# Performance work log

Measured on AMD Instinct MI355X. Metric: run time of the kernel, lower is better.

## Reference

```python
import jax, jax.numpy as jnp
import numpy as np

N, E, D = 40000, 640000, 128
EPS = 1e-5


def _lin(k, out_d, in_d):
    s = 1.0 / np.sqrt(in_d)
    kw, kb = jax.random.split(k)
    W = jax.random.uniform(kw, (out_d, in_d), minval=-s, maxval=s, dtype=jnp.float32)
    b = jax.random.uniform(kb, (out_d,), minval=-s, maxval=s, dtype=jnp.float32)
    return W, b


def setup_inputs() -> dict:
    key = jax.random.key(0)
    kx, ke, k1, k2, k3, k4 = jax.random.split(key, 6)
    x = jax.random.normal(kx, (N, D), dtype=jnp.float32)
    edge_index = jax.random.randint(ke, (2, E), 0, N, dtype=jnp.int64)
    Wm1, bm1 = _lin(k1, D, D)
    Wm2, bm2 = _lin(k2, D, D)
    Wu1, bu1 = _lin(k3, D, 2 * D)
    Wu2, bu2 = _lin(k4, D, D)
    gamma = jnp.ones((D,), jnp.float32)
    beta = jnp.zeros((D,), jnp.float32)
    return dict(x=x, edge_index=edge_index, Wm1=Wm1, bm1=bm1, Wm2=Wm2, bm2=bm2,
                Wu1=Wu1, bu1=bu1, Wu2=Wu2, bu2=bu2, gamma=gamma, beta=beta)


def reference(x, edge_index, Wm1, bm1, Wm2, bm2, Wu1, bu1, Wu2, bu2, gamma, beta):
    num_nodes = x.shape[0]
    src, dst = edge_index[0], edge_index[1]
    # message MLP on gathered source features: (E, D)
    m = jax.nn.relu(x[src] @ Wm1.T + bm1) @ Wm2.T + bm2
    # scatter-mean via segment_sum + clamped count
    agg = jax.ops.segment_sum(m, dst, num_segments=num_nodes)
    cnt = jax.ops.segment_sum(jnp.ones((dst.shape[0],), m.dtype), dst, num_segments=num_nodes)
    agg = agg / jnp.clip(cnt, 1.0, None)[:, None]
    # update MLP on concat([x, agg]) -> (N, D); dropout is identity in eval
    comb = jnp.concatenate([x, agg], axis=-1)
    u = jax.nn.relu(comb @ Wu1.T + bu1) @ Wu2.T + bu2
    # residual + LayerNorm
    h = u + x
    mu = h.mean(-1, keepdims=True)
    var = ((h - mu) ** 2).mean(-1, keepdims=True)
    return (h - mu) / jnp.sqrt(var + EPS) * gamma + beta
```

## Files before the change

kernel.cpp:

```cpp
#include <hip/hip_runtime.h>

#define N_NODES 40000
#define N_EDGES 640000
#define DIM 128
#define PAD 32
#define NBLK 625
#define SCAT_BLOCKS 625

typedef __bf16 bf16;
typedef __bf16 v8bf __attribute__((ext_vector_type(8)));
typedef __bf16 v4bf __attribute__((ext_vector_type(4)));
typedef float f32x4 __attribute__((ext_vector_type(4)));

#define MFMA(a, b, c) __builtin_amdgcn_mfma_f32_16x16x32_bf16(a, b, c, 0, 0, 0)

#define OFF_WM1 0
#define OFF_BM1 16384
#define OFF_WM2 16512
#define OFF_BM2 32896
#define OFF_WU1 33024
#define OFF_BU1 65792
#define OFF_WU2 65920
#define OFF_BU2 82304
#define OFF_GAM 82432
#define OFF_BET 82560
#define NPARAM  82688

__device__ __forceinline__ void detect(const void* x, const void* ei,
                                       int* sf, int& f32m, int& i64m) {
    const int tid = threadIdx.x;
    if (tid == 0) { sf[0] = 0; sf[1] = 0; }
    __syncthreads();
    const unsigned short* xh = (const unsigned short*)x;
    const unsigned int* eiw = (const unsigned int*)ei;
    int isf32 = 0; unsigned int orhi = 0;
    #pragma unroll
    for (int j = 0; j < 4; ++j) {
        unsigned short h = xh[2 * (tid + 256 * j)];
        if (((h >> 7) & 0xFF) >= 0xC0) isf32 = 1;
        orhi |= eiw[2 * (tid + 256 * j) + 1];
    }
    if (isf32) atomicOr(&sf[0], 1);
    if (orhi)  atomicOr(&sf[1], 1);
    __syncthreads();
    f32m = sf[0];
    i64m = sf[1] ? 0 : 1;
}

__global__ __launch_bounds__(256) void scatter_kernel(
    const void* __restrict__ x, const void* __restrict__ ei,
    const void* p0, const void* p1, const void* p2, const void* p3,
    const void* p4, const void* p5, const void* p6, const void* p7,
    const void* p8, const void* p9,
    int* __restrict__ cnt8, unsigned short* __restrict__ pad8,
    bf16* __restrict__ xb, bf16* __restrict__ wp, int* __restrict__ flags)
{
    __shared__ int sf[2];
    int f32m, i64m;
    detect(x, ei, sf, f32m, i64m);
    const int gid = blockIdx.x * 256 + threadIdx.x;
    const int gstride = SCAT_BLOCKS * 256;
    const int cls = blockIdx.x & 7;
    if (gid == 0) { flags[0] = f32m; flags[1] = i64m; }

    int s[4], d[4];
    if (i64m) {
        const long long* p = (const long long*)ei;
        int e0 = gid * 4;
        #pragma unroll
        for (int j = 0; j < 4; ++j) { s[j] = (int)p[e0 + j]; d[j] = (int)p[N_EDGES + e0 + j]; }
    } else {
        const int4* ps = (const int4*)ei;
        const int4* pd = ps + N_EDGES / 4;
        int4 sv = ps[gid], dv = pd[gid];
        s[0] = sv.x; s[1] = sv.y; s[2] = sv.z; s[3] = sv.w;
        d[0] = dv.x; d[1] = dv.y; d[2] = dv.z; d[3] = dv.w;
    }
    int pos[4];
    #pragma unroll
    for (int j = 0; j < 4; ++j) pos[j] = atomicAdd(&cnt8[cls * N_NODES + d[j]], 1);
    #pragma unroll
    for (int j = 0; j < 4; ++j)
        if (pos[j] < PAD)
            pad8[(((size_t)cls * N_NODES + d[j]) << 5) + pos[j]] = (unsigned short)s[j];

    const int NT = N_NODES * DIM;
    if (f32m) {
        const float4* g = (const float4*)x;
        v4bf* o = (v4bf*)xb;
        for (int i = gid; i < NT / 4; i += gstride) {
            float4 v = g[i];
            v4bf t; t[0] = (bf16)v.x; t[1] = (bf16)v.y; t[2] = (bf16)v.z; t[3] = (bf16)v.w;
            o[i] = t;
        }
    } else {
        const uint4* g = (const uint4*)x;
        uint4* o = (uint4*)xb;
        for (int i = gid; i < NT / 8; i += gstride) o[i] = g[i];
    }
    for (int i = gid; i < NPARAM; i += gstride) {
        const void* src; int base;
        if      (i < OFF_BM1) { src = p0; base = OFF_WM1; }
        else if (i < OFF_WM2) { src = p1; base = OFF_BM1; }
        else if (i < OFF_BM2) { src = p2; base = OFF_WM2; }
        else if (i < OFF_WU1) { src = p3; base = OFF_BM2; }
        else if (i < OFF_BU1) { src = p4; base = OFF_WU1; }
        else if (i < OFF_WU2) { src = p5; base = OFF_BU1; }
        else if (i < OFF_BU2) { src = p6; base = OFF_WU2; }
        else if (i < OFF_GAM) { src = p7; base = OFF_BU2; }
        else if (i < OFF_BET) { src = p8; base = OFF_GAM; }
        else                  { src = p9; base = OFF_BET; }
        int j = i - base;
        float v = f32m ? ((const float*)src)[j] : (float)((const bf16*)src)[j];
        wp[i] = (bf16)v;
    }
}

__global__ __launch_bounds__(256) void msg_kernel(const bf16* __restrict__ xb,
                                                  const bf16* __restrict__ wp,
                                                  bf16* __restrict__ y)
{
    __shared__ __align__(16) bf16 sc[4][16 * DIM];
    const int wave = threadIdx.x >> 6, lane = threadIdx.x & 63;
    const int l15 = lane & 15, quad = lane >> 4;
    const int row0 = (blockIdx.x * 4 + wave) * 16;
    bf16* s = sc[wave];
    const size_t ra = (size_t)(row0 + l15) * DIM;

    f32x4 acc[8] = {};
    #pragma unroll
    for (int kt = 0; kt < 4; ++kt) {
        int k0 = kt * 32 + quad * 8;
        v8bf a0 = *(const v8bf*)&xb[ra + k0];
        #pragma unroll
        for (int ct = 0; ct < 8; ++ct) {
            v8bf b = *(const v8bf*)&wp[OFF_WM1 + (size_t)(ct * 16 + l15) * DIM + k0];
            acc[ct] = MFMA(a0, b, acc[ct]);
        }
    }
    #pragma unroll
    for (int ct = 0; ct < 8; ++ct) {
        float bb = (float)wp[OFF_BM1 + ct * 16 + l15];
        int c8w = (ct << 1) | (l15 >> 3);
        #pragma unroll
        for (int r = 0; r < 4; ++r) {
            int row = quad * 4 + r;
            s[row * DIM + (((c8w ^ row) << 3) | (l15 & 7))] =
                (bf16)fmaxf(acc[ct][r] + bb, 0.f);
        }
    }
    f32x4 acc2[8] = {};
    #pragma unroll
    for (int kt = 0; kt < 4; ++kt) {
        int k0 = kt * 32 + quad * 8;
        int c8 = kt * 4 + quad;
        v8bf a0 = *(const v8bf*)&s[l15 * DIM + ((c8 ^ l15) << 3)];
        #pragma unroll
        for (int ct = 0; ct < 8; ++ct) {
            v8bf b = *(const v8bf*)&wp[OFF_WM2 + (size_t)(ct * 16 + l15) * DIM + k0];
            acc2[ct] = MFMA(a0, b, acc2[ct]);
        }
    }
    #pragma unroll
    for (int ct = 0; ct < 8; ++ct) {
        float bb = (float)wp[OFF_BM2 + ct * 16 + l15];
        #pragma unroll
        for (int r = 0; r < 4; ++r) {
            int grow = row0 + quad * 4 + r;
            y[(size_t)grow * DIM + ct * 16 + l15] = (bf16)(acc2[ct][r] + bb);
        }
    }
}

__device__ __forceinline__ void accum8(float* s, uint4 v) {
    v8bf b = __builtin_bit_cast(v8bf, v);
    #pragma unroll
    for (int j = 0; j < 8; ++j) s[j] += (float)b[j];
}

__global__ __launch_bounds__(256) void update_kernel(
    const bf16* __restrict__ xb, const bf16* __restrict__ y,
    const unsigned short* __restrict__ pad8, const int* __restrict__ cnt8,
    const bf16* __restrict__ wp, const int* __restrict__ flags,
    void* __restrict__ out)
{
    __shared__ __align__(16) bf16 sA[4][16 * DIM];
    __shared__ __align__(16) bf16 sH[4][16 * DIM];
    const int wave = threadIdx.x >> 6, lane = threadIdx.x & 63;
    const int l15 = lane & 15, quad = lane >> 4;
    const int row0 = (blockIdx.x * 4 + wave) * 16;
    bf16* sa = sA[wave];
    bf16* s  = sH[wave];
    const int of32 = flags[0];
    const uint4* yv = (const uint4*)y;

    for (int idx = 0; idx < 16; ++idx) {
        const int node = row0 + idx;
        int pref[9];
        pref[0] = 0;
        #pragma unroll
        for (int xq = 0; xq < 8; ++xq)
            pref[xq + 1] = pref[xq] + min(cnt8[xq * N_NODES + node], PAD);
        const int tot = pref[8];

        float s0[8] = {}, s1[8] = {};
        int j = quad;
        for (; j + 4 < tot; j += 8) {
            int j2 = j + 4, x1 = 0, x2 = 0;
            #pragma unroll
            for (int xq = 1; xq < 8; ++xq) {
                if (j  >= pref[xq]) x1 = xq;
                if (j2 >= pref[xq]) x2 = xq;
            }
            int i0 = pad8[(((size_t)x1 * N_NODES + node) << 5) + (j  - pref[x1])];
            int i1 = pad8[(((size_t)x2 * N_NODES + node) << 5) + (j2 - pref[x2])];
            uint4 v0 = yv[(size_t)i0 * 16 + l15];
            uint4 v1 = yv[(size_t)i1 * 16 + l15];
            accum8(s0, v0);
            accum8(s1, v1);
        }
        if (j < tot) {
            int x1 = 0;
            #pragma unroll
            for (int xq = 1; xq < 8; ++xq) if (j >= pref[xq]) x1 = xq;
            int i0 = pad8[(((size_t)x1 * N_NODES + node) << 5) + (j - pref[x1])];
            accum8(s0, yv[(size_t)i0 * 16 + l15]);
        }
        float inv = 1.f / (float)(tot > 0 ? tot : 1);
        v8bf o;
        #pragma unroll
        for (int jj = 0; jj < 8; ++jj) {
            float v = s0[jj] + s1[jj];
            v += __shfl_xor(v, 16);
            v += __shfl_xor(v, 32);
            o[jj] = (bf16)(v * inv);
        }
        if (quad == 0)
            *(v8bf*)&sa[idx * DIM + (((l15 ^ idx) << 3))] = o;
    }

    const size_t ra = (size_t)(row0 + l15) * DIM;
    f32x4 acc[8] = {};
    #pragma unroll
    for (int kt = 0; kt < 8; ++kt) {
        int k0 = kt * 32 + quad * 8;
        v8bf a0;
        if (kt < 4) {
            a0 = *(const v8bf*)&xb[ra + k0];
        } else {
            int c8 = (kt - 4) * 4 + quad;
            a0 = *(const v8bf*)&sa[l15 * DIM + ((c8 ^ l15) << 3)];
        }
        #pragma unroll
        for (int ct = 0; ct < 8; ++ct) {
            v8bf b = *(const v8bf*)&wp[OFF_WU1 + (size_t)(ct * 16 + l15) * 256 + k0];
            acc[ct] = MFMA(a0, b, acc[ct]);
        }
    }
    #pragma unroll
    for (int ct = 0; ct < 8; ++ct) {
        float bb = (float)wp[OFF_BU1 + ct * 16 + l15];
        int c8w = (ct << 1) | (l15 >> 3);
        #pragma unroll
        for (int r = 0; r < 4; ++r) {
            int row = quad * 4 + r;
            s[row * DIM + (((c8w ^ row) << 3) | (l15 & 7))] =
                (bf16)fmaxf(acc[ct][r] + bb, 0.f);
        }
    }
    f32x4 acc2[8] = {};
    #pragma unroll
    for (int kt = 0; kt < 4; ++kt) {
        int k0 = kt * 32 + quad * 8;
        int c8 = kt * 4 + quad;
        v8bf a0 = *(const v8bf*)&s[l15 * DIM + ((c8 ^ l15) << 3)];
        #pragma unroll
        for (int ct = 0; ct < 8; ++ct) {
            v8bf b = *(const v8bf*)&wp[OFF_WU2 + (size_t)(ct * 16 + l15) * DIM + k0];
            acc2[ct] = MFMA(a0, b, acc2[ct]);
        }
    }

    float bu2c[8], gc[8], bc[8];
    #pragma unroll
    for (int ct = 0; ct < 8; ++ct) {
        int col = ct * 16 + l15;
        bu2c[ct] = (float)wp[OFF_BU2 + col];
        gc[ct]   = (float)wp[OFF_GAM + col];
        bc[ct]   = (float)wp[OFF_BET + col];
    }
    #pragma unroll
    for (int r = 0; r < 4; ++r) {
        int grow = row0 + quad * 4 + r;
        float u[8], s1 = 0.f, s2 = 0.f;
        #pragma unroll
        for (int ct = 0; ct < 8; ++ct) {
            float v = acc2[ct][r] + bu2c[ct]
                    + (float)xb[(size_t)grow * DIM + ct * 16 + l15];
            u[ct] = v; s1 += v; s2 += v * v;
        }
        #pragma unroll
        for (int off = 1; off < 16; off <<= 1) {
            s1 += __shfl_xor(s1, off);
            s2 += __shfl_xor(s2, off);
        }
        float mean = s1 * (1.f / 128.f);
        float var  = s2 * (1.f / 128.f) - mean * mean;
        float rstd = rsqrtf(var + 1e-5f);
        if (of32) {
            #pragma unroll
            for (int ct = 0; ct < 8; ++ct)
                ((float*)out)[(size_t)grow * DIM + ct * 16 + l15] =
                    (u[ct] - mean) * rstd * gc[ct] + bc[ct];
        } else {
            #pragma unroll
            for (int ct = 0; ct < 8; ++ct)
                ((bf16*)out)[(size_t)grow * DIM + ct * 16 + l15] =
                    (bf16)((u[ct] - mean) * rstd * gc[ct] + bc[ct]);
        }
    }
}

extern "C" void kernel_launch(void* const* d_in, const int* in_sizes, int n_in,
                              void* d_out, int out_size, void* d_ws, size_t ws_size,
                              hipStream_t stream) {
    const void* x  = d_in[0];
    const void* ei = d_in[1];

    char* ws = (char*)d_ws;
    size_t off = 0;
    auto alloc = [&](size_t bytes) {
        void* p = ws + off;
        off += (bytes + 255) & ~(size_t)255;
        return p;
    };
    bf16* y    = (bf16*)alloc((size_t)N_NODES * DIM * sizeof(bf16));
    bf16* xb   = (bf16*)alloc((size_t)N_NODES * DIM * sizeof(bf16));
    bf16* wp   = (bf16*)alloc((size_t)NPARAM * sizeof(bf16));
    int*  cnt8 = (int*)alloc((size_t)8 * N_NODES * sizeof(int));
    unsigned short* pad8 =
        (unsigned short*)alloc((size_t)8 * N_NODES * PAD * sizeof(unsigned short));
    int* flags = (int*)alloc(256);

    hipMemsetAsync(cnt8, 0, (size_t)8 * N_NODES * sizeof(int), stream);

    scatter_kernel<<<SCAT_BLOCKS, 256, 0, stream>>>(
        x, ei, d_in[2], d_in[3], d_in[4], d_in[5], d_in[6], d_in[7],
        d_in[8], d_in[9], d_in[10], d_in[11], cnt8, pad8, xb, wp, flags);
    msg_kernel<<<NBLK, 256, 0, stream>>>(xb, wp, y);
    update_kernel<<<NBLK, 256, 0, stream>>>(xb, y, pad8, cnt8, wp, flags, d_out);
}
```

Before: 232.2 us.

## Split neighbor aggregation into its own kernel with one wave per node

Moves the gather-mean aggregation out of the update kernel into a separate agg_kernel that launches 10000 blocks, one wave per node, and writes the aggregated features to a global bf16 buffer. Before, each wave in update_kernel walked its 16 nodes one after another, which serialized the latency-bound gathers and left few waves to hide memory latency. The update kernel now reads agg straight from global memory and keeps only one LDS buffer. The cost is an extra launch and an extra global write and read of the 40000x128 bf16 aggregate.

```diff
diff --git a/kernel.cpp b/kernel.cpp
--- a/kernel.cpp
+++ b/kernel.cpp
@@ -178,79 +178,78 @@
     for (int j = 0; j < 8; ++j) s[j] += (float)b[j];
 }
 
+__global__ __launch_bounds__(256) void agg_kernel(const bf16* __restrict__ y,
+                                                  const unsigned short* __restrict__ pad8,
+                                                  const int* __restrict__ cnt8,
+                                                  bf16* __restrict__ agg) {
+    const int node = (blockIdx.x << 2) + (threadIdx.x >> 6);
+    const int lane = threadIdx.x & 63;
+    const int slot = lane >> 4, c16 = lane & 15;
+    const uint4* yv = (const uint4*)y;
+
+    int pref[9];
+    pref[0] = 0;
+    #pragma unroll
+    for (int xq = 0; xq < 8; ++xq)
+        pref[xq + 1] = pref[xq] + min(cnt8[xq * N_NODES + node], PAD);
+    const int tot = pref[8];
+
+    float s0[8] = {}, s1[8] = {};
+    int j = slot;
+    for (; j + 4 < tot; j += 8) {
+        int j2 = j + 4, x1 = 0, x2 = 0;
+        #pragma unroll
+        for (int xq = 1; xq < 8; ++xq) {
+            if (j  >= pref[xq]) x1 = xq;
+            if (j2 >= pref[xq]) x2 = xq;
+        }
+        int i0 = pad8[(((size_t)x1 * N_NODES + node) << 5) + (j  - pref[x1])];
+        int i1 = pad8[(((size_t)x2 * N_NODES + node) << 5) + (j2 - pref[x2])];
+        uint4 v0 = yv[(size_t)i0 * 16 + c16];
+        uint4 v1 = yv[(size_t)i1 * 16 + c16];
+        accum8(s0, v0);
+        accum8(s1, v1);
+    }
+    if (j < tot) {
+        int x1 = 0;
+        #pragma unroll
+        for (int xq = 1; xq < 8; ++xq) if (j >= pref[xq]) x1 = xq;
+        int i0 = pad8[(((size_t)x1 * N_NODES + node) << 5) + (j - pref[x1])];
+        accum8(s0, yv[(size_t)i0 * 16 + c16]);
+    }
+
+    float inv = 1.f / (float)(tot > 0 ? tot : 1);
+    v8bf o;
+    #pragma unroll
+    for (int jj = 0; jj < 8; ++jj) {
+        float v = s0[jj] + s1[jj];
+        v += __shfl_xor(v, 16);
+        v += __shfl_xor(v, 32);
+        o[jj] = (bf16)(v * inv);
+    }
+    if (slot == 0)
+        ((uint4*)agg)[(size_t)node * 16 + c16] = __builtin_bit_cast(uint4, o);
+}
+
 __global__ __launch_bounds__(256) void update_kernel(
-    const bf16* __restrict__ xb, const bf16* __restrict__ y,
-    const unsigned short* __restrict__ pad8, const int* __restrict__ cnt8,
+    const bf16* __restrict__ xb, const bf16* __restrict__ agg,
     const bf16* __restrict__ wp, const int* __restrict__ flags,
     void* __restrict__ out)
 {
-    __shared__ __align__(16) bf16 sA[4][16 * DIM];
-    __shared__ __align__(16) bf16 sH[4][16 * DIM];
+    __shared__ __align__(16) bf16 sc[4][16 * DIM];
     const int wave = threadIdx.x >> 6, lane = threadIdx.x & 63;
     const int l15 = lane & 15, quad = lane >> 4;
     const int row0 = (blockIdx.x * 4 + wave) * 16;
-    bf16* sa = sA[wave];
-    bf16* s  = sH[wave];
+    bf16* s = sc[wave];
+    const size_t ra = (size_t)(row0 + l15) * DIM;
     const int of32 = flags[0];
-    const uint4* yv = (const uint4*)y;
-
-    for (int idx = 0; idx < 16; ++idx) {
-        const int node = row0 + idx;
-        int pref[9];
-        pref[0] = 0;
-        #pragma unroll
-        for (int xq = 0; xq < 8; ++xq)
-            pref[xq + 1] = pref[xq] + min(cnt8[xq * N_NODES + node], PAD);
-        const int tot = pref[8];
-
-        float s0[8] = {}, s1[8] = {};
-        int j = quad;
-        for (; j + 4 < tot; j += 8) {
-            int j2 = j + 4, x1 = 0, x2 = 0;
-            #pragma unroll
-            for (int xq = 1; xq < 8; ++xq) {
-                if (j  >= pref[xq]) x1 = xq;
-                if (j2 >= pref[xq]) x2 = xq;
-            }
-            int i0 = pad8[(((size_t)x1 * N_NODES + node) << 5) + (j  - pref[x1])];
-            int i1 = pad8[(((size_t)x2 * N_NODES + node) << 5) + (j2 - pref[x2])];
-            uint4 v0 = yv[(size_t)i0 * 16 + l15];
-            uint4 v1 = yv[(size_t)i1 * 16 + l15];
-            accum8(s0, v0);
-            accum8(s1, v1);
-        }
-        if (j < tot) {
-            int x1 = 0;
-            #pragma unroll
-            for (int xq = 1; xq < 8; ++xq) if (j >= pref[xq]) x1 = xq;
-            int i0 = pad8[(((size_t)x1 * N_NODES + node) << 5) + (j - pref[x1])];
-            accum8(s0, yv[(size_t)i0 * 16 + l15]);
-        }
-        float inv = 1.f / (float)(tot > 0 ? tot : 1);
-        v8bf o;
-        #pragma unroll
-        for (int jj = 0; jj < 8; ++jj) {
-            float v = s0[jj] + s1[jj];
-            v += __shfl_xor(v, 16);
-            v += __shfl_xor(v, 32);
-            o[jj] = (bf16)(v * inv);
-        }
-        if (quad == 0)
-            *(v8bf*)&sa[idx * DIM + (((l15 ^ idx) << 3))] = o;
-    }
-
-    const size_t ra = (size_t)(row0 + l15) * DIM;
+
     f32x4 acc[8] = {};
     #pragma unroll
     for (int kt = 0; kt < 8; ++kt) {
         int k0 = kt * 32 + quad * 8;
-        v8bf a0;
-        if (kt < 4) {
-            a0 = *(const v8bf*)&xb[ra + k0];
-        } else {
-            int c8 = (kt - 4) * 4 + quad;
-            a0 = *(const v8bf*)&sa[l15 * DIM + ((c8 ^ l15) << 3)];
-        }
+        v8bf a0 = (kt < 4) ? *(const v8bf*)&xb[ra + k0]
+                           : *(const v8bf*)&agg[ra + (k0 - 128)];
         #pragma unroll
         for (int ct = 0; ct < 8; ++ct) {
             v8bf b = *(const v8bf*)&wp[OFF_WU1 + (size_t)(ct * 16 + l15) * 256 + k0];
@@ -335,6 +334,7 @@
         return p;
     };
     bf16* y    = (bf16*)alloc((size_t)N_NODES * DIM * sizeof(bf16));
+    bf16* agg  = (bf16*)alloc((size_t)N_NODES * DIM * sizeof(bf16));
     bf16* xb   = (bf16*)alloc((size_t)N_NODES * DIM * sizeof(bf16));
     bf16* wp   = (bf16*)alloc((size_t)NPARAM * sizeof(bf16));
     int*  cnt8 = (int*)alloc((size_t)8 * N_NODES * sizeof(int));
@@ -348,5 +348,6 @@
         x, ei, d_in[2], d_in[3], d_in[4], d_in[5], d_in[6], d_in[7],
         d_in[8], d_in[9], d_in[10], d_in[11], cnt8, pad8, xb, wp, flags);
     msg_kernel<<<NBLK, 256, 0, stream>>>(xb, wp, y);
-    update_kernel<<<NBLK, 256, 0, stream>>>(xb, y, pad8, cnt8, wp, flags, d_out);
-}
+    agg_kernel<<<N_NODES / 4, 256, 0, stream>>>(y, pad8, cnt8, agg);
+    update_kernel<<<NBLK, 256, 0, stream>>>(xb, agg, wp, flags, d_out);
+}
```

Result: faster. 219.1 us (-5.6%).
